# Performance work log

Hardware: AMD Instinct MI355X
Metric: run time of the kernel (lower is better)

The kernel has to match this reference:

```python
import jax, jax.numpy as jnp
import numpy as np
from jax.scipy.special import logsumexp

# K particles, J proposal candidates, N taxa, R merges done, T current subtrees,
# S sites, A alphabet, D embedding dim
K, J, N, R, T, S, A, D = 128, 4, 64, 32, 32, 256, 4, 64
PRIOR_BL = 0.1       # expected branch length under exponential prior
TEMPERATURE = 1.0


def _gather_nodes(arr, idx):
    # arr: (Z, t, ...); idx: (Z,) -> (Z, ...)  (per-row gather, gather_K)
    i = idx.reshape((-1,) + (1,) * (arr.ndim - 1))
    return jnp.take_along_axis(arr, i, axis=1)[:, 0]


def _replace_with_merged(arr, idx1, idx2, new_val):
    # remove nodes idx1, idx2 from each row (keeping order) and append merged node
    t = arr.shape[1]
    pos = jnp.arange(t)
    removed = (pos[None, :] == idx1[:, None]) | (pos[None, :] == idx2[:, None])
    order = jnp.argsort(removed.astype(jnp.int32), axis=1, stable=True)
    kept = order[:, : t - 2]
    ki = kept.reshape(kept.shape + (1,) * (arr.ndim - 2))
    kept_vals = jnp.take_along_axis(arr, ki, axis=1)
    return jnp.concatenate([kept_vals, new_val[:, None]], axis=1)


def _hash_tree(h1, h2):
    # order-invariant int32 hash combine (wraps on overflow, as intended)
    mn = jnp.minimum(h1, h2)
    mx = jnp.maximum(h1, h2)
    return (mn * 1000003 + mx) * 40503 + 2531011


def _q_matrix(emb_ZxD, W_q):
    # GTR-style rate matrix from merged-node embedding (site-independent decoder)
    logits = (emb_ZxD @ W_q).reshape(-1, A, A)
    off = jax.nn.softplus(logits) * (1.0 - jnp.eye(A, dtype=logits.dtype))
    return off - jnp.eye(A, dtype=logits.dtype) * off.sum(-1, keepdims=True)


def setup_inputs() -> dict:
    key = jax.random.key(0)
    ks = jax.random.split(key, 20)
    merge1_indexes_Kxr = jax.random.randint(ks[0], (K, R), 0, N).astype(jnp.int32)
    merge2_indexes_Kxr = jax.random.randint(ks[1], (K, R), 0, N).astype(jnp.int32)
    branch1_lengths_Kxr = jax.random.uniform(ks[2], (K, R)) * 0.2 + 1e-3
    branch2_lengths_Kxr = jax.random.uniform(ks[3], (K, R)) * 0.2 + 1e-3
    embeddings_KxrxD = jax.random.normal(ks[4], (K, R, D))
    # leaf counts per subtree, summing to N per particle
    lc_row = jnp.concatenate([jnp.full((T // 2,), 1, jnp.int32), jnp.full((T - T // 2,), 3, jnp.int32)])
    leaf_counts_Kxt = jnp.tile(lc_row[None], (K, 1))
    hashes_Kxt = jax.random.randint(ks[5], (K, T), 0, 2 ** 30).astype(jnp.int32)
    embeddings_KxtxD = jax.random.normal(ks[6], (K, T, D))
    log_felsensteins_KxtxSxA = -jax.random.uniform(ks[7], (K, T, S, A)) * 3.0
    log_pi_K = -jax.random.uniform(ks[8], (K,)) * 100.0
    indexes_K = jax.random.randint(ks[9], (K,), 0, K).astype(jnp.int32)
    # proposal outputs (stand-in for the learned proposal): idx1 != idx2
    idx1_KxJ = jax.random.randint(ks[10], (K, J), 0, T).astype(jnp.int32)
    off = jax.random.randint(ks[11], (K, J), 1, T).astype(jnp.int32)
    idx2_KxJ = (idx1_KxJ + off) % T
    branch1_KxJ = jax.random.uniform(ks[12], (K, J)) * 0.2 + 1e-3
    branch2_KxJ = jax.random.uniform(ks[13], (K, J)) * 0.2 + 1e-3
    embedding_KxJxD = jax.random.normal(ks[14], (K, J, D))
    log_v_plus_KxJ = jnp.full((K, J), np.log(T * (T - 1) / 2.0), jnp.float32)
    gumbel_KxJ = jax.random.gumbel(ks[15], (K, J))
    W_q = jax.random.normal(ks[16], (D, A * A)) * 0.05
    W_stat = jax.random.normal(ks[17], (D, A)) * 0.05
    vals = np.zeros(2 * N, dtype=np.float64)
    for i in range(2, 2 * N):
        vals[i] = vals[i - 2] + np.log(i)
    log_double_factorials_2N = jnp.asarray(vals, jnp.float32)
    return {
        'indexes_K': indexes_K,
        'merge1_indexes_Kxr': merge1_indexes_Kxr,
        'merge2_indexes_Kxr': merge2_indexes_Kxr,
        'branch1_lengths_Kxr': branch1_lengths_Kxr,
        'branch2_lengths_Kxr': branch2_lengths_Kxr,
        'embeddings_KxrxD': embeddings_KxrxD,
        'leaf_counts_Kxt': leaf_counts_Kxt,
        'hashes_Kxt': hashes_Kxt,
        'embeddings_KxtxD': embeddings_KxtxD,
        'log_felsensteins_KxtxSxA': log_felsensteins_KxtxSxA,
        'log_pi_K': log_pi_K,
        'idx1_KxJ': idx1_KxJ,
        'idx2_KxJ': idx2_KxJ,
        'branch1_KxJ': branch1_KxJ,
        'branch2_KxJ': branch2_KxJ,
        'embedding_KxJxD': embedding_KxJxD,
        'log_v_plus_KxJ': log_v_plus_KxJ,
        'gumbel_KxJ': gumbel_KxJ,
        'W_q': W_q,
        'W_stat': W_stat,
        'log_double_factorials_2N': log_double_factorials_2N,
    }


def reference(indexes_K, merge1_indexes_Kxr, merge2_indexes_Kxr,
              branch1_lengths_Kxr, branch2_lengths_Kxr, embeddings_KxrxD,
              leaf_counts_Kxt, hashes_Kxt, embeddings_KxtxD,
              log_felsensteins_KxtxSxA, log_pi_K,
              idx1_KxJ, idx2_KxJ, branch1_KxJ, branch2_KxJ,
              embedding_KxJxD, log_v_plus_KxJ, gumbel_KxJ,
              W_q, W_stat, log_double_factorials_2N):
    # ---- ancestor resampling gather (ms[...][indexes_K]) ----
    g = lambda a: a[indexes_K]
    merge1_Kxr = g(merge1_indexes_Kxr); merge2_Kxr = g(merge2_indexes_Kxr)
    b1_Kxr = g(branch1_lengths_Kxr); b2_Kxr = g(branch2_lengths_Kxr)
    emb_KxrxD = g(embeddings_KxrxD)
    lc_Kxt = g(leaf_counts_Kxt); h_Kxt = g(hashes_Kxt)
    emb_KxtxD = g(embeddings_KxtxD)
    lf_KxtxSxA = g(log_felsensteins_KxtxSxA)
    logpi_K = g(log_pi_K)
    # ---- flatten proposal to Z = K*J (hash_trick=False: Z = K*J, no dedup) ----
    Z = K * J
    rep = lambda a: jnp.repeat(a, J, axis=0)  # K_to_Z
    idx1_Z = idx1_KxJ.reshape(Z); idx2_Z = idx2_KxJ.reshape(Z)
    branch1_Z = branch1_KxJ.reshape(Z); branch2_Z = branch2_KxJ.reshape(Z)
    emb_ZxD = embedding_KxJxD.reshape(Z, D)
    log_v_plus_Z = log_v_plus_KxJ.reshape(Z)
    merge1_Z = rep(merge1_Kxr); merge2_Z = rep(merge2_Kxr)
    b1_Z = rep(b1_Kxr); b2_Z = rep(b2_Kxr)
    embr_Z = rep(emb_KxrxD)
    lc_Z = rep(lc_Kxt); h_Z = rep(h_Kxt)
    embt_Z = rep(emb_KxtxD)
    lf_Z = rep(lf_KxtxSxA)
    logpi_Z = rep(logpi_K)
    # ---- append candidate branches ----
    b1_all = jnp.concatenate([b1_Z, branch1_Z[:, None]], axis=1)  # Z x (R+1)
    b2_all = jnp.concatenate([b2_Z, branch2_Z[:, None]], axis=1)
    # ---- merge step ----
    new_lc = _gather_nodes(lc_Z, idx1_Z) + _gather_nodes(lc_Z, idx2_Z)
    new_h = _hash_tree(_gather_nodes(h_Z, idx1_Z), _gather_nodes(h_Z, idx2_Z))
    lc_new = _replace_with_merged(lc_Z, idx1_Z, idx2_Z, new_lc)      # Z x (T-1)
    h_new = _replace_with_merged(h_Z, idx1_Z, idx2_Z, new_h)
    embt_new = _replace_with_merged(embt_Z, idx1_Z, idx2_Z, emb_ZxD)
    # ---- Felsenstein pruning update ----
    Q = _q_matrix(emb_ZxD, W_q)                                      # Z x A x A
    expm = jax.scipy.linalg.expm
    P1 = jax.vmap(expm)(Q * branch1_Z[:, None, None])
    P2 = jax.vmap(expm)(Q * branch2_Z[:, None, None])
    logP1 = jnp.log(jnp.clip(P1, 1e-30))
    logP2 = jnp.log(jnp.clip(P2, 1e-30))
    lf1 = _gather_nodes(lf_Z, idx1_Z)  # Z x S x A
    lf2 = _gather_nodes(lf_Z, idx2_Z)
    new_lf = (logsumexp(logP1[:, None, :, :] + lf1[:, :, None, :], axis=-1)
              + logsumexp(logP2[:, None, :, :] + lf2[:, :, None, :], axis=-1))
    lf_new = _replace_with_merged(lf_Z, idx1_Z, idx2_Z, new_lf)      # Z x (T-1) x S x A
    # ---- stationary probs per node & log pi ----
    log_stat = jax.nn.log_softmax(embt_new @ W_stat, axis=-1)        # Z x (T-1) x A
    ll_nodes = logsumexp(lf_new + log_stat[:, :, None, :], axis=-1).sum(-1)  # Z x (T-1)
    log_lik_Z = ll_nodes.sum(-1)
    rate = 1.0 / PRIOR_BL
    log_branch_prior = ((jnp.log(rate) - rate * b1_all).sum(-1)
                        + (jnp.log(rate) - rate * b2_all).sum(-1))
    df_idx = jnp.clip(2 * lc_new - 3, 0, 2 * N - 1)
    log_topo = -log_double_factorials_2N[df_idx].sum(-1)
    log_pi_new_Z = log_lik_Z + log_branch_prior + log_topo
    log_v_minus_Z = jnp.log(jnp.sum(lc_new > 1, axis=-1).astype(jnp.float32))
    # ---- weights & sub-resampling ----
    log_w_Z = log_pi_new_Z - logpi_Z + log_v_minus_Z - log_v_plus_Z
    log_w_KxJ = log_w_Z.reshape(K, J)
    log_weight_K = logsumexp(log_w_KxJ, axis=1) - jnp.log(float(J))
    sub_idx_K = jnp.argmax(log_w_KxJ / TEMPERATURE + gumbel_KxJ, axis=1)  # Gumbel-max = Categorical sample
    sel = jnp.arange(K) * J + sub_idx_K
    gs = lambda a: a[sel]
    merge1_out = jnp.concatenate([gs(merge1_Z), gs(idx1_Z)[:, None]], axis=1)
    merge2_out = jnp.concatenate([gs(merge2_Z), gs(idx2_Z)[:, None]], axis=1)
    embr_out = jnp.concatenate([gs(embr_Z), gs(emb_ZxD)[:, None, :]], axis=1)
    return (merge1_out, merge2_out, gs(b1_all), gs(b2_all), embr_out,
            gs(lc_new), gs(h_new), gs(embt_new), gs(lf_new),
            gs(log_pi_new_Z), log_weight_K, gs(log_lik_Z))
```

## Files before the change

### kernel.cpp

```cpp
#include <hip/hip_runtime.h>
#include <math.h>

constexpr int K_ = 128, J_ = 4, R_ = 32, T_ = 32, S_ = 256, A_ = 4, D_ = 64;
constexpr int NDF_ = 128;
constexpr float RATE_ = 10.0f;

constexpr int OFF_M1   = 0;
constexpr int OFF_M2   = OFF_M1 + K_ * 33;
constexpr int OFF_B1   = OFF_M2 + K_ * 33;
constexpr int OFF_B2   = OFF_B1 + K_ * 33;
constexpr int OFF_EMBR = OFF_B2 + K_ * 33;
constexpr int OFF_LC   = OFF_EMBR + K_ * 33 * D_;
constexpr int OFF_H    = OFF_LC + K_ * 31;
constexpr int OFF_EMBT = OFF_H + K_ * 31;
constexpr int OFF_LF   = OFF_EMBT + K_ * 31 * D_;
constexpr int OFF_LPN  = OFF_LF + K_ * 31 * S_ * A_;
constexpr int OFF_LW   = OFF_LPN + K_;
constexpr int OFF_LL   = OFF_LW + K_;

__device__ inline float lse4f(float a, float b, float c, float d) {
    float m = fmaxf(fmaxf(a, b), fmaxf(c, d));
    return m + __logf(__expf(a - m) + __expf(b - m) + __expf(c - m) + __expf(d - m));
}

__global__ __launch_bounds__(256) void k_all(
    const int* __restrict__ indexes, const int* __restrict__ m1_Kr,
    const int* __restrict__ m2_Kr, const float* __restrict__ b1_Kr,
    const float* __restrict__ b2_Kr, const float* __restrict__ embr,
    const int* __restrict__ lc_Kt, const int* __restrict__ h_Kt,
    const float* __restrict__ embt, const float* __restrict__ lf,
    const float* __restrict__ logpi_K, const int* __restrict__ idx1_KJ,
    const int* __restrict__ idx2_KJ, const float* __restrict__ br1_KJ,
    const float* __restrict__ br2_KJ, const float* __restrict__ emb_KJD,
    const float* __restrict__ logvp_KJ, const float* __restrict__ gumbel_KJ,
    const float* __restrict__ Wq, const float* __restrict__ Wstat,
    const float* __restrict__ ldf, float* __restrict__ out) {
    int k = blockIdx.x;
    int tid = threadIdx.x;
    int w = tid >> 6, lane = tid & 63;
    int src = indexes[k];

    __shared__ float s_node_ll[T_];
    __shared__ float s_new_ll[J_];
    __shared__ float s_logP[J_][32];
    __shared__ int s_sub;

#pragma unroll
    for (int i = 0; i < 8; ++i) {
        int t = i * 4 + w;
        float e = embt[(src * T_ + t) * D_ + lane];
        const float4 w4 = *(const float4*)&Wstat[lane * 4];
        float g0 = e * w4.x, g1 = e * w4.y, g2 = e * w4.z, g3 = e * w4.w;
#pragma unroll
        for (int m = 32; m; m >>= 1) {
            g0 += __shfl_xor(g0, m, 64);
            g1 += __shfl_xor(g1, m, 64);
            g2 += __shfl_xor(g2, m, 64);
            g3 += __shfl_xor(g3, m, 64);
        }
        float lse = lse4f(g0, g1, g2, g3);
        float ls0 = g0 - lse, ls1 = g1 - lse, ls2 = g2 - lse, ls3 = g3 - lse;
        const float4* fr = (const float4*)&lf[(size_t)(src * T_ + t) * S_ * A_];
        double acc = 0.0;
#pragma unroll
        for (int s4 = 0; s4 < 4; ++s4) {
            float4 f = fr[s4 * 64 + lane];
            acc += (double)lse4f(f.x + ls0, f.y + ls1, f.z + ls2, f.w + ls3);
        }
#pragma unroll
        for (int m = 32; m; m >>= 1) acc += __shfl_xor(acc, m, 64);
        if (lane == 0) s_node_ll[t] = (float)acc;
    }

    {
        int z = k * J_ + w;
        int i1 = idx1_KJ[z], i2 = idx2_KJ[z];

        float emb_d = emb_KJD[z * D_ + lane];
        float lg[20];
        const float4* wqr = (const float4*)&Wq[lane * 16];
        float4 q0 = wqr[0], q1 = wqr[1], q2 = wqr[2], q3 = wqr[3];
        lg[0] = emb_d * q0.x;  lg[1] = emb_d * q0.y;  lg[2] = emb_d * q0.z;  lg[3] = emb_d * q0.w;
        lg[4] = emb_d * q1.x;  lg[5] = emb_d * q1.y;  lg[6] = emb_d * q1.z;  lg[7] = emb_d * q1.w;
        lg[8] = emb_d * q2.x;  lg[9] = emb_d * q2.y;  lg[10] = emb_d * q2.z; lg[11] = emb_d * q2.w;
        lg[12] = emb_d * q3.x; lg[13] = emb_d * q3.y; lg[14] = emb_d * q3.z; lg[15] = emb_d * q3.w;
        const float4 ws4 = *(const float4*)&Wstat[lane * 4];
        lg[16] = emb_d * ws4.x; lg[17] = emb_d * ws4.y; lg[18] = emb_d * ws4.z; lg[19] = emb_d * ws4.w;
#pragma unroll
        for (int m = 32; m; m >>= 1) {
#pragma unroll
            for (int p = 0; p < 20; ++p) lg[p] += __shfl_xor(lg[p], m, 64);
        }

        float lseS = lse4f(lg[16], lg[17], lg[18], lg[19]);
        float ls0 = lg[16] - lseS, ls1 = lg[17] - lseS, ls2 = lg[18] - lseS, ls3 = lg[19] - lseS;

        float lv[4] = {0.f, 0.f, 0.f, 0.f};
        if (lane < 8) {
            int h = lane >> 2, r = lane & 3, base = h * 4;
            float q[16];
#pragma unroll
            for (int i = 0; i < 4; ++i) {
                float rs = 0.f;
#pragma unroll
                for (int j = 0; j < 4; ++j) {
                    if (i != j) {
                        float x = lg[i * 4 + j];
                        float sp = (x > 15.f) ? x : log1pf(__expf(x));
                        q[i * 4 + j] = sp;
                        rs += sp;
                    }
                }
                q[i * 4 + i] = -rs;
            }
            float br = (h == 0) ? br1_KJ[z] : br2_KJ[z];
            float c = br * (1.f / 64.f);
#pragma unroll
            for (int e2 = 0; e2 < 16; ++e2) q[e2] *= c;
            float trow[4], arow[4];
#pragma unroll
            for (int j = 0; j < 4; ++j) { trow[j] = (j == r) ? 1.f : 0.f; arow[j] = trow[j]; }
            const float inv_n[11] = {0.f, 1.f, 0.5f, 1.f / 3.f, 0.25f, 0.2f,
                                     1.f / 6.f, 1.f / 7.f, 0.125f, 1.f / 9.f, 0.1f};
#pragma unroll
            for (int n = 1; n <= 10; ++n) {
                float nt[4];
#pragma unroll
                for (int j = 0; j < 4; ++j)
                    nt[j] = (trow[0] * q[0 * 4 + j] + trow[1] * q[1 * 4 + j] +
                             trow[2] * q[2 * 4 + j] + trow[3] * q[3 * 4 + j]) * inv_n[n];
#pragma unroll
                for (int j = 0; j < 4; ++j) { trow[j] = nt[j]; arow[j] += nt[j]; }
            }
#pragma unroll
            for (int sq = 0; sq < 6; ++sq) {
                float nrow[4];
#pragma unroll
                for (int j = 0; j < 4; ++j) {
                    float aj = arow[j];
                    nrow[j] = arow[0] * __shfl(aj, base + 0, 64)
                            + arow[1] * __shfl(aj, base + 1, 64)
                            + arow[2] * __shfl(aj, base + 2, 64)
                            + arow[3] * __shfl(aj, base + 3, 64);
                }
#pragma unroll
                for (int j = 0; j < 4; ++j) arow[j] = nrow[j];
            }
#pragma unroll
            for (int j = 0; j < 4; ++j) {
                lv[j] = __logf(fmaxf(arow[j], 1e-30f));
                s_logP[w][h * 16 + r * 4 + j] = lv[j];
            }
        }
        float p1[16], p2[16];
#pragma unroll
        for (int r = 0; r < 4; ++r) {
#pragma unroll
            for (int j = 0; j < 4; ++j) {
                p1[r * 4 + j] = __shfl(lv[j], r, 64);
                p2[r * 4 + j] = __shfl(lv[j], 4 + r, 64);
            }
        }
        const float4* f1p = (const float4*)&lf[(size_t)(src * T_ + i1) * S_ * A_];
        const float4* f2p = (const float4*)&lf[(size_t)(src * T_ + i2) * S_ * A_];
        double acc = 0.0;
#pragma unroll
        for (int s4 = 0; s4 < 4; ++s4) {
            float4 f = f1p[s4 * 64 + lane];
            float4 g = f2p[s4 * 64 + lane];
            float nlf[4];
#pragma unroll
            for (int a = 0; a < 4; ++a) {
                float t1 = lse4f(p1[a * 4 + 0] + f.x, p1[a * 4 + 1] + f.y,
                                 p1[a * 4 + 2] + f.z, p1[a * 4 + 3] + f.w);
                float t2 = lse4f(p2[a * 4 + 0] + g.x, p2[a * 4 + 1] + g.y,
                                 p2[a * 4 + 2] + g.z, p2[a * 4 + 3] + g.w);
                nlf[a] = t1 + t2;
            }
            acc += (double)lse4f(nlf[0] + ls0, nlf[1] + ls1, nlf[2] + ls2, nlf[3] + ls3);
        }
#pragma unroll
        for (int m = 32; m; m >>= 1) acc += __shfl_xor(acc, m, 64);
        if (lane == 0) s_new_ll[w] = (float)acc;
    }
    __syncthreads();

    if (w == 0) {
        double nll = 0.0, topo = 0.0, sb1 = 0.0, sb2 = 0.0;
        int cnt = 0;
        if (lane < T_) {
            nll = (double)s_node_ll[lane];
            int lc = lc_Kt[src * T_ + lane];
            int di = 2 * lc - 3; di = max(0, min(NDF_ - 1, di));
            topo = (double)ldf[di];
            cnt = (lc > 1) ? 1 : 0;
            sb1 = (double)b1_Kr[src * R_ + lane];
            sb2 = (double)b2_Kr[src * R_ + lane];
        }
        for (int o = 32; o > 0; o >>= 1) {
            nll += __shfl_down(nll, o, 64);
            topo += __shfl_down(topo, o, 64);
            sb1 += __shfl_down(sb1, o, 64);
            sb2 += __shfl_down(sb2, o, 64);
            cnt += __shfl_down(cnt, o, 64);
        }
        if (lane == 0) {
            double total_ll = nll, base_topo = -topo;
            const double lr = log(10.0);
            double lw[4], lpn[4], llik[4];
            for (int j = 0; j < J_; ++j) {
                int z = k * J_ + j;
                int i1 = idx1_KJ[z], i2 = idx2_KJ[z];
                int lc1 = lc_Kt[src * T_ + i1], lc2 = lc_Kt[src * T_ + i2];
                int nlc = lc1 + lc2;
                double loglik = total_ll - (double)s_node_ll[i1] - (double)s_node_ll[i2]
                              + (double)s_new_ll[j];
                double lbp = 66.0 * lr
                           - (double)RATE_ * (sb1 + (double)br1_KJ[z] + sb2 + (double)br2_KJ[z]);
                int d1 = max(0, min(NDF_ - 1, 2 * lc1 - 3));
                int d2 = max(0, min(NDF_ - 1, 2 * lc2 - 3));
                int dn = max(0, min(NDF_ - 1, 2 * nlc - 3));
                double lt = base_topo + (double)ldf[d1] + (double)ldf[d2] - (double)ldf[dn];
                int cntj = cnt - ((lc1 > 1) ? 1 : 0) - ((lc2 > 1) ? 1 : 0) + 1;
                double lvm = log((double)cntj);
                lpn[j] = loglik + lbp + lt;
                llik[j] = loglik;
                lw[j] = lpn[j] - (double)logpi_K[src] + lvm - (double)logvp_KJ[z];
            }
            double m = fmax(fmax(lw[0], lw[1]), fmax(lw[2], lw[3]));
            double ssum = exp(lw[0] - m) + exp(lw[1] - m) + exp(lw[2] - m) + exp(lw[3] - m);
            double logw = m + log(ssum) - log((double)J_);
            int best = 0;
            double bv = lw[0] + (double)gumbel_KJ[k * J_ + 0];
            for (int j = 1; j < J_; ++j) {
                double v = lw[j] + (double)gumbel_KJ[k * J_ + j];
                if (v > bv) { bv = v; best = j; }
            }
            out[OFF_LPN + k] = (float)lpn[best];
            out[OFF_LW + k] = (float)logw;
            out[OFF_LL + k] = (float)llik[best];
            s_sub = best;
        }
    }
    __syncthreads();

    int sub = s_sub;
    int zs = k * J_ + sub;
    int si1 = idx1_KJ[zs], si2 = idx2_KJ[zs];
    int mn = min(si1, si2), mx = max(si1, si2);

    {
        float P1[16], P2[16];
#pragma unroll
        for (int i = 0; i < 16; ++i) { P1[i] = s_logP[sub][i]; P2[i] = s_logP[sub][16 + i]; }
        const float4 f1 = *(const float4*)&lf[((size_t)(src * T_ + si1) * S_ + tid) * A_];
        const float4 f2 = *(const float4*)&lf[((size_t)(src * T_ + si2) * S_ + tid) * A_];
        float4 o4;
#pragma unroll
        for (int a = 0; a < 4; ++a) {
            float t1 = lse4f(P1[a * 4 + 0] + f1.x, P1[a * 4 + 1] + f1.y,
                             P1[a * 4 + 2] + f1.z, P1[a * 4 + 3] + f1.w);
            float t2 = lse4f(P2[a * 4 + 0] + f2.x, P2[a * 4 + 1] + f2.y,
                             P2[a * 4 + 2] + f2.z, P2[a * 4 + 3] + f2.w);
            ((float*)&o4)[a] = t1 + t2;
        }
        *(float4*)&out[OFF_LF + ((size_t)(k * 31 + 30) * S_ + tid) * A_] = o4;
    }
    for (int row = 0; row < 30; ++row) {
        int st = row;
        if (st >= mn) ++st;
        if (st >= mx) ++st;
        const float4 v = *(const float4*)&lf[((size_t)(src * T_ + st) * S_ + tid) * A_];
        *(float4*)&out[OFF_LF + ((size_t)(k * 31 + row) * S_ + tid) * A_] = v;
    }
    for (int i = tid; i < 33; i += 256) {
        float v1, v2, fb1, fb2;
        if (i < 32) {
            v1 = (float)m1_Kr[src * R_ + i];
            v2 = (float)m2_Kr[src * R_ + i];
            fb1 = b1_Kr[src * R_ + i];
            fb2 = b2_Kr[src * R_ + i];
        } else {
            v1 = (float)si1; v2 = (float)si2;
            fb1 = br1_KJ[zs]; fb2 = br2_KJ[zs];
        }
        out[OFF_M1 + k * 33 + i] = v1;
        out[OFF_M2 + k * 33 + i] = v2;
        out[OFF_B1 + k * 33 + i] = fb1;
        out[OFF_B2 + k * 33 + i] = fb2;
    }
    for (int i = tid; i < 33 * D_; i += 256) {
        int r = i >> 6, d = i & 63;
        float v = (r < 32) ? embr[(src * R_ + r) * D_ + d] : emb_KJD[zs * D_ + d];
        out[OFF_EMBR + k * 33 * D_ + i] = v;
    }
    for (int i = tid; i < 31; i += 256) {
        int lcv, hv;
        if (i < 30) {
            int st = i;
            if (st >= mn) ++st;
            if (st >= mx) ++st;
            lcv = lc_Kt[src * T_ + st];
            hv = h_Kt[src * T_ + st];
        } else {
            lcv = lc_Kt[src * T_ + si1] + lc_Kt[src * T_ + si2];
            int h1 = h_Kt[src * T_ + si1], h2 = h_Kt[src * T_ + si2];
            int hmn = min(h1, h2), hmx = max(h1, h2);
            unsigned int u = ((unsigned int)hmn * 1000003u + (unsigned int)hmx) * 40503u
                             + 2531011u;
            hv = (int)u;
        }
        out[OFF_LC + k * 31 + i] = (float)lcv;
        out[OFF_H + k * 31 + i] = (float)hv;
    }
    for (int i = tid; i < 31 * D_; i += 256) {
        int t = i >> 6, d = i & 63;
        float v;
        if (t < 30) {
            int st = t;
            if (st >= mn) ++st;
            if (st >= mx) ++st;
            v = embt[(src * T_ + st) * D_ + d];
        } else {
            v = emb_KJD[zs * D_ + d];
        }
        out[OFF_EMBT + k * 31 * D_ + i] = v;
    }
}

extern "C" void kernel_launch(void* const* d_in, const int* in_sizes, int n_in,
                              void* d_out, int out_size, void* d_ws, size_t ws_size,
                              hipStream_t stream) {
    const int* indexes   = (const int*)d_in[0];
    const int* m1_Kr     = (const int*)d_in[1];
    const int* m2_Kr     = (const int*)d_in[2];
    const float* b1_Kr   = (const float*)d_in[3];
    const float* b2_Kr   = (const float*)d_in[4];
    const float* embr    = (const float*)d_in[5];
    const int* lc_Kt     = (const int*)d_in[6];
    const int* h_Kt      = (const int*)d_in[7];
    const float* embt    = (const float*)d_in[8];
    const float* lf      = (const float*)d_in[9];
    const float* logpi_K = (const float*)d_in[10];
    const int* idx1_KJ   = (const int*)d_in[11];
    const int* idx2_KJ   = (const int*)d_in[12];
    const float* br1_KJ  = (const float*)d_in[13];
    const float* br2_KJ  = (const float*)d_in[14];
    const float* emb_KJD = (const float*)d_in[15];
    const float* logvp_KJ = (const float*)d_in[16];
    const float* gumbel_KJ = (const float*)d_in[17];
    const float* Wq      = (const float*)d_in[18];
    const float* Wstat   = (const float*)d_in[19];
    const float* ldf     = (const float*)d_in[20];
    float* out = (float*)d_out;

    k_all<<<K_, 256, 0, stream>>>(indexes, m1_Kr, m2_Kr, b1_Kr, b2_Kr, embr,
                                  lc_Kt, h_Kt, embt, lf, logpi_K, idx1_KJ, idx2_KJ,
                                  br1_KJ, br2_KJ, emb_KJD, logvp_KJ, gumbel_KJ,
                                  Wq, Wstat, ldf, out);
}
```

Baseline: 146.2 us.

## Split fused per-particle kernel into compute, finalize, and copy kernels with wider grids

Replaces the single 128-block kernel with three launches. A 9xK-block compute kernel spreads the node log-likelihoods and candidate evaluations across blocks and writes them to workspace. A small finalize kernel does the weight and Gumbel selection, and a 9xK-block copy kernel writes the gathered outputs with float4 accesses. The aim is to fill more compute units than the 128 blocks the old version used on a large GPU, at the cost of two extra launches and round trips through global workspace.

```diff
diff --git a/kernel.cpp b/kernel.cpp
--- a/kernel.cpp
+++ b/kernel.cpp
@@ -18,36 +18,30 @@
 constexpr int OFF_LW   = OFF_LPN + K_;
 constexpr int OFF_LL   = OFF_LW + K_;
 
+constexpr int WS_NODE  = 0;
+constexpr int WS_NEWLL = WS_NODE + K_ * T_;
+constexpr int WS_LOGP  = WS_NEWLL + K_ * J_;
+constexpr int WS_SUB   = WS_LOGP + K_ * J_ * 32;
+
 __device__ inline float lse4f(float a, float b, float c, float d) {
     float m = fmaxf(fmaxf(a, b), fmaxf(c, d));
     return m + __logf(__expf(a - m) + __expf(b - m) + __expf(c - m) + __expf(d - m));
 }
 
-__global__ __launch_bounds__(256) void k_all(
-    const int* __restrict__ indexes, const int* __restrict__ m1_Kr,
-    const int* __restrict__ m2_Kr, const float* __restrict__ b1_Kr,
-    const float* __restrict__ b2_Kr, const float* __restrict__ embr,
-    const int* __restrict__ lc_Kt, const int* __restrict__ h_Kt,
-    const float* __restrict__ embt, const float* __restrict__ lf,
-    const float* __restrict__ logpi_K, const int* __restrict__ idx1_KJ,
+__global__ __launch_bounds__(256) void k_compute(
+    const int* __restrict__ indexes, const float* __restrict__ embt,
+    const float* __restrict__ lf, const float* __restrict__ Wstat,
+    const float* __restrict__ Wq, const int* __restrict__ idx1_KJ,
     const int* __restrict__ idx2_KJ, const float* __restrict__ br1_KJ,
     const float* __restrict__ br2_KJ, const float* __restrict__ emb_KJD,
-    const float* __restrict__ logvp_KJ, const float* __restrict__ gumbel_KJ,
-    const float* __restrict__ Wq, const float* __restrict__ Wstat,
-    const float* __restrict__ ldf, float* __restrict__ out) {
-    int k = blockIdx.x;
-    int tid = threadIdx.x;
-    int w = tid >> 6, lane = tid & 63;
+    float* __restrict__ ws) {
+    int grp = blockIdx.x;
+    int k = blockIdx.y;
+    int tid = threadIdx.x, w = tid >> 6, lane = tid & 63;
     int src = indexes[k];
 
-    __shared__ float s_node_ll[T_];
-    __shared__ float s_new_ll[J_];
-    __shared__ float s_logP[J_][32];
-    __shared__ int s_sub;
-
-#pragma unroll
-    for (int i = 0; i < 8; ++i) {
-        int t = i * 4 + w;
+    if (grp < 8) {
+        int t = grp * 4 + w;
         float e = embt[(src * T_ + t) * D_ + lane];
         const float4 w4 = *(const float4*)&Wstat[lane * 4];
         float g0 = e * w4.x, g1 = e * w4.y, g2 = e * w4.z, g3 = e * w4.w;
@@ -69,10 +63,8 @@
         }
 #pragma unroll
         for (int m = 32; m; m >>= 1) acc += __shfl_xor(acc, m, 64);
-        if (lane == 0) s_node_ll[t] = (float)acc;
-    }
-
-    {
+        if (lane == 0) ws[WS_NODE + k * T_ + t] = (float)acc;
+    } else {
         int z = k * J_ + w;
         int i1 = idx1_KJ[z], i2 = idx2_KJ[z];
 
@@ -149,7 +141,7 @@
 #pragma unroll
             for (int j = 0; j < 4; ++j) {
                 lv[j] = __logf(fmaxf(arow[j], 1e-30f));
-                s_logP[w][h * 16 + r * 4 + j] = lv[j];
+                ws[WS_LOGP + z * 32 + h * 16 + r * 4 + j] = lv[j];
             }
         }
         float p1[16], p2[16];
@@ -167,113 +159,104 @@
 #pragma unroll
         for (int s4 = 0; s4 < 4; ++s4) {
             float4 f = f1p[s4 * 64 + lane];
-            float4 g = f2p[s4 * 64 + lane];
+            float4 f2v = f2p[s4 * 64 + lane];
             float nlf[4];
 #pragma unroll
             for (int a = 0; a < 4; ++a) {
                 float t1 = lse4f(p1[a * 4 + 0] + f.x, p1[a * 4 + 1] + f.y,
                                  p1[a * 4 + 2] + f.z, p1[a * 4 + 3] + f.w);
-                float t2 = lse4f(p2[a * 4 + 0] + g.x, p2[a * 4 + 1] + g.y,
-                                 p2[a * 4 + 2] + g.z, p2[a * 4 + 3] + g.w);
+                float t2 = lse4f(p2[a * 4 + 0] + f2v.x, p2[a * 4 + 1] + f2v.y,
+                                 p2[a * 4 + 2] + f2v.z, p2[a * 4 + 3] + f2v.w);
                 nlf[a] = t1 + t2;
             }
             acc += (double)lse4f(nlf[0] + ls0, nlf[1] + ls1, nlf[2] + ls2, nlf[3] + ls3);
         }
 #pragma unroll
         for (int m = 32; m; m >>= 1) acc += __shfl_xor(acc, m, 64);
-        if (lane == 0) s_new_ll[w] = (float)acc;
-    }
-    __syncthreads();
-
-    if (w == 0) {
-        double nll = 0.0, topo = 0.0, sb1 = 0.0, sb2 = 0.0;
-        int cnt = 0;
-        if (lane < T_) {
-            nll = (double)s_node_ll[lane];
-            int lc = lc_Kt[src * T_ + lane];
-            int di = 2 * lc - 3; di = max(0, min(NDF_ - 1, di));
-            topo = (double)ldf[di];
-            cnt = (lc > 1) ? 1 : 0;
-            sb1 = (double)b1_Kr[src * R_ + lane];
-            sb2 = (double)b2_Kr[src * R_ + lane];
-        }
-        for (int o = 32; o > 0; o >>= 1) {
-            nll += __shfl_down(nll, o, 64);
-            topo += __shfl_down(topo, o, 64);
-            sb1 += __shfl_down(sb1, o, 64);
-            sb2 += __shfl_down(sb2, o, 64);
-            cnt += __shfl_down(cnt, o, 64);
-        }
-        if (lane == 0) {
-            double total_ll = nll, base_topo = -topo;
-            const double lr = log(10.0);
-            double lw[4], lpn[4], llik[4];
-            for (int j = 0; j < J_; ++j) {
-                int z = k * J_ + j;
-                int i1 = idx1_KJ[z], i2 = idx2_KJ[z];
-                int lc1 = lc_Kt[src * T_ + i1], lc2 = lc_Kt[src * T_ + i2];
-                int nlc = lc1 + lc2;
-                double loglik = total_ll - (double)s_node_ll[i1] - (double)s_node_ll[i2]
-                              + (double)s_new_ll[j];
-                double lbp = 66.0 * lr
-                           - (double)RATE_ * (sb1 + (double)br1_KJ[z] + sb2 + (double)br2_KJ[z]);
-                int d1 = max(0, min(NDF_ - 1, 2 * lc1 - 3));
-                int d2 = max(0, min(NDF_ - 1, 2 * lc2 - 3));
-                int dn = max(0, min(NDF_ - 1, 2 * nlc - 3));
-                double lt = base_topo + (double)ldf[d1] + (double)ldf[d2] - (double)ldf[dn];
-                int cntj = cnt - ((lc1 > 1) ? 1 : 0) - ((lc2 > 1) ? 1 : 0) + 1;
-                double lvm = log((double)cntj);
-                lpn[j] = loglik + lbp + lt;
-                llik[j] = loglik;
-                lw[j] = lpn[j] - (double)logpi_K[src] + lvm - (double)logvp_KJ[z];
-            }
-            double m = fmax(fmax(lw[0], lw[1]), fmax(lw[2], lw[3]));
-            double ssum = exp(lw[0] - m) + exp(lw[1] - m) + exp(lw[2] - m) + exp(lw[3] - m);
-            double logw = m + log(ssum) - log((double)J_);
-            int best = 0;
-            double bv = lw[0] + (double)gumbel_KJ[k * J_ + 0];
-            for (int j = 1; j < J_; ++j) {
-                double v = lw[j] + (double)gumbel_KJ[k * J_ + j];
-                if (v > bv) { bv = v; best = j; }
-            }
-            out[OFF_LPN + k] = (float)lpn[best];
-            out[OFF_LW + k] = (float)logw;
-            out[OFF_LL + k] = (float)llik[best];
-            s_sub = best;
-        }
-    }
-    __syncthreads();
-
-    int sub = s_sub;
-    int zs = k * J_ + sub;
+        if (lane == 0) ws[WS_NEWLL + z] = (float)acc;
+    }
+}
+
+__global__ __launch_bounds__(64) void k_finalize(
+    const int* __restrict__ indexes, const int* __restrict__ m1_Kr,
+    const int* __restrict__ m2_Kr, const float* __restrict__ b1_Kr,
+    const float* __restrict__ b2_Kr, const int* __restrict__ lc_Kt,
+    const int* __restrict__ h_Kt, const float* __restrict__ logpi_K,
+    const int* __restrict__ idx1_KJ, const int* __restrict__ idx2_KJ,
+    const float* __restrict__ br1_KJ, const float* __restrict__ br2_KJ,
+    const float* __restrict__ logvp_KJ, const float* __restrict__ gumbel_KJ,
+    const float* __restrict__ ldf, float* __restrict__ ws, float* __restrict__ out) {
+    int k = blockIdx.x;
+    int lane = threadIdx.x;
+    int src = indexes[k];
+
+    double nll = 0.0, topo = 0.0, sb1 = 0.0, sb2 = 0.0;
+    int cnt = 0;
+    if (lane < T_) {
+        nll = (double)ws[WS_NODE + k * T_ + lane];
+        int lc = lc_Kt[src * T_ + lane];
+        int di = 2 * lc - 3; di = max(0, min(NDF_ - 1, di));
+        topo = (double)ldf[di];
+        cnt = (lc > 1) ? 1 : 0;
+        sb1 = (double)b1_Kr[src * R_ + lane];
+        sb2 = (double)b2_Kr[src * R_ + lane];
+    }
+    for (int o = 32; o > 0; o >>= 1) {
+        nll += __shfl_down(nll, o, 64);
+        topo += __shfl_down(topo, o, 64);
+        sb1 += __shfl_down(sb1, o, 64);
+        sb2 += __shfl_down(sb2, o, 64);
+        cnt += __shfl_down(cnt, o, 64);
+    }
+    nll = __shfl(nll, 0, 64); topo = __shfl(topo, 0, 64);
+    sb1 = __shfl(sb1, 0, 64); sb2 = __shfl(sb2, 0, 64);
+    cnt = __shfl(cnt, 0, 64);
+    double total_ll = nll, base_topo = -topo;
+    const double lr = log(10.0);
+
+    double lwj = 0.0, lpnj = 0.0, llikj = 0.0;
+    if (lane < J_) {
+        int j = lane, z = k * J_ + j;
+        int i1 = idx1_KJ[z], i2 = idx2_KJ[z];
+        int lc1 = lc_Kt[src * T_ + i1], lc2 = lc_Kt[src * T_ + i2];
+        int nlc = lc1 + lc2;
+        double loglik = total_ll - (double)ws[WS_NODE + k * T_ + i1]
+                      - (double)ws[WS_NODE + k * T_ + i2] + (double)ws[WS_NEWLL + z];
+        double lbp = 66.0 * lr
+                   - (double)RATE_ * (sb1 + (double)br1_KJ[z] + sb2 + (double)br2_KJ[z]);
+        int d1 = max(0, min(NDF_ - 1, 2 * lc1 - 3));
+        int d2 = max(0, min(NDF_ - 1, 2 * lc2 - 3));
+        int dn = max(0, min(NDF_ - 1, 2 * nlc - 3));
+        double lt = base_topo + (double)ldf[d1] + (double)ldf[d2] - (double)ldf[dn];
+        int cntj = cnt - ((lc1 > 1) ? 1 : 0) - ((lc2 > 1) ? 1 : 0) + 1;
+        double lvm = log((double)cntj);
+        lpnj = loglik + lbp + lt;
+        llikj = loglik;
+        lwj = lpnj - (double)logpi_K[src] + lvm - (double)logvp_KJ[z];
+    }
+    double lw0 = __shfl(lwj, 0, 64), lw1 = __shfl(lwj, 1, 64);
+    double lw2 = __shfl(lwj, 2, 64), lw3 = __shfl(lwj, 3, 64);
+    double m = fmax(fmax(lw0, lw1), fmax(lw2, lw3));
+    double ssum = exp(lw0 - m) + exp(lw1 - m) + exp(lw2 - m) + exp(lw3 - m);
+    double logw = m + log(ssum) - log((double)J_);
+    int best = 0;
+    double bv = lw0 + (double)gumbel_KJ[k * J_ + 0];
+    { double v = lw1 + (double)gumbel_KJ[k * J_ + 1]; if (v > bv) { bv = v; best = 1; } }
+    { double v = lw2 + (double)gumbel_KJ[k * J_ + 2]; if (v > bv) { bv = v; best = 2; } }
+    { double v = lw3 + (double)gumbel_KJ[k * J_ + 3]; if (v > bv) { bv = v; best = 3; } }
+    double lpn_b = __shfl(lpnj, best, 64);
+    double llik_b = __shfl(llikj, best, 64);
+    if (lane == 0) {
+        out[OFF_LPN + k] = (float)lpn_b;
+        out[OFF_LW + k] = (float)logw;
+        out[OFF_LL + k] = (float)llik_b;
+        ((int*)(ws + WS_SUB))[k] = best;
+    }
+
+    int zs = k * J_ + best;
     int si1 = idx1_KJ[zs], si2 = idx2_KJ[zs];
     int mn = min(si1, si2), mx = max(si1, si2);
-
-    {
-        float P1[16], P2[16];
-#pragma unroll
-        for (int i = 0; i < 16; ++i) { P1[i] = s_logP[sub][i]; P2[i] = s_logP[sub][16 + i]; }
-        const float4 f1 = *(const float4*)&lf[((size_t)(src * T_ + si1) * S_ + tid) * A_];
-        const float4 f2 = *(const float4*)&lf[((size_t)(src * T_ + si2) * S_ + tid) * A_];
-        float4 o4;
-#pragma unroll
-        for (int a = 0; a < 4; ++a) {
-            float t1 = lse4f(P1[a * 4 + 0] + f1.x, P1[a * 4 + 1] + f1.y,
-                             P1[a * 4 + 2] + f1.z, P1[a * 4 + 3] + f1.w);
-            float t2 = lse4f(P2[a * 4 + 0] + f2.x, P2[a * 4 + 1] + f2.y,
-                             P2[a * 4 + 2] + f2.z, P2[a * 4 + 3] + f2.w);
-            ((float*)&o4)[a] = t1 + t2;
-        }
-        *(float4*)&out[OFF_LF + ((size_t)(k * 31 + 30) * S_ + tid) * A_] = o4;
-    }
-    for (int row = 0; row < 30; ++row) {
-        int st = row;
-        if (st >= mn) ++st;
-        if (st >= mx) ++st;
-        const float4 v = *(const float4*)&lf[((size_t)(src * T_ + st) * S_ + tid) * A_];
-        *(float4*)&out[OFF_LF + ((size_t)(k * 31 + row) * S_ + tid) * A_] = v;
-    }
-    for (int i = tid; i < 33; i += 256) {
+    for (int i = lane; i < 33; i += 64) {
         float v1, v2, fb1, fb2;
         if (i < 32) {
             v1 = (float)m1_Kr[src * R_ + i];
@@ -289,12 +272,7 @@
         out[OFF_B1 + k * 33 + i] = fb1;
         out[OFF_B2 + k * 33 + i] = fb2;
     }
-    for (int i = tid; i < 33 * D_; i += 256) {
-        int r = i >> 6, d = i & 63;
-        float v = (r < 32) ? embr[(src * R_ + r) * D_ + d] : emb_KJD[zs * D_ + d];
-        out[OFF_EMBR + k * 33 * D_ + i] = v;
-    }
-    for (int i = tid; i < 31; i += 256) {
+    for (int i = lane; i < 31; i += 64) {
         int lcv, hv;
         if (i < 30) {
             int st = i;
@@ -313,18 +291,77 @@
         out[OFF_LC + k * 31 + i] = (float)lcv;
         out[OFF_H + k * 31 + i] = (float)hv;
     }
-    for (int i = tid; i < 31 * D_; i += 256) {
-        int t = i >> 6, d = i & 63;
-        float v;
-        if (t < 30) {
-            int st = t;
-            if (st >= mn) ++st;
-            if (st >= mx) ++st;
-            v = embt[(src * T_ + st) * D_ + d];
-        } else {
-            v = emb_KJD[zs * D_ + d];
-        }
-        out[OFF_EMBT + k * 31 * D_ + i] = v;
+}
+
+__global__ __launch_bounds__(256) void k_copy(
+    const int* __restrict__ indexes, const int* __restrict__ idx1_KJ,
+    const int* __restrict__ idx2_KJ, const float* __restrict__ embr,
+    const float* __restrict__ embt, const float* __restrict__ lf,
+    const float* __restrict__ emb_KJD, const float* __restrict__ ws,
+    float* __restrict__ out) {
+    int grp = blockIdx.x;
+    int k = blockIdx.y;
+    int tid = threadIdx.x;
+    int src = indexes[k];
+    int sub = ((const int*)(ws + WS_SUB))[k];
+    int zs = k * J_ + sub;
+    int si1 = idx1_KJ[zs], si2 = idx2_KJ[zs];
+    int mn = min(si1, si2), mx = max(si1, si2);
+
+    if (grp < 8) {
+        __shared__ float sP[32];
+        if (grp == 7) {
+            if (tid < 32) sP[tid] = ws[WS_LOGP + zs * 32 + tid];
+            __syncthreads();
+        }
+#pragma unroll
+        for (int rr = 0; rr < 4; ++rr) {
+            int row = grp * 4 + rr;
+            if (row >= 31) break;
+            if (row < 30) {
+                int st = row;
+                if (st >= mn) ++st;
+                if (st >= mx) ++st;
+                const float4 v = *(const float4*)&lf[((size_t)(src * T_ + st) * S_ + tid) * A_];
+                *(float4*)&out[OFF_LF + ((size_t)(k * 31 + row) * S_ + tid) * A_] = v;
+            } else {
+                float P1[16], P2[16];
+#pragma unroll
+                for (int i = 0; i < 16; ++i) { P1[i] = sP[i]; P2[i] = sP[16 + i]; }
+                const float4 f1 = *(const float4*)&lf[((size_t)(src * T_ + si1) * S_ + tid) * A_];
+                const float4 f2 = *(const float4*)&lf[((size_t)(src * T_ + si2) * S_ + tid) * A_];
+                float4 o4;
+#pragma unroll
+                for (int a = 0; a < 4; ++a) {
+                    float t1 = lse4f(P1[a * 4 + 0] + f1.x, P1[a * 4 + 1] + f1.y,
+                                     P1[a * 4 + 2] + f1.z, P1[a * 4 + 3] + f1.w);
+                    float t2 = lse4f(P2[a * 4 + 0] + f2.x, P2[a * 4 + 1] + f2.y,
+                                     P2[a * 4 + 2] + f2.z, P2[a * 4 + 3] + f2.w);
+                    ((float*)&o4)[a] = t1 + t2;
+                }
+                *(float4*)&out[OFF_LF + ((size_t)(k * 31 + 30) * S_ + tid) * A_] = o4;
+            }
+        }
+    } else {
+        for (int i = tid; i < 33 * 16; i += 256) {
+            int r = i >> 4, c = i & 15;
+            float4 v = (r < 32) ? *(const float4*)&embr[(src * R_ + r) * D_ + c * 4]
+                                : *(const float4*)&emb_KJD[zs * D_ + c * 4];
+            *(float4*)&out[OFF_EMBR + k * 33 * D_ + i * 4] = v;
+        }
+        for (int i = tid; i < 31 * 16; i += 256) {
+            int t = i >> 4, c = i & 15;
+            float4 v;
+            if (t < 30) {
+                int st = t;
+                if (st >= mn) ++st;
+                if (st >= mx) ++st;
+                v = *(const float4*)&embt[(src * T_ + st) * D_ + c * 4];
+            } else {
+                v = *(const float4*)&emb_KJD[zs * D_ + c * 4];
+            }
+            *(float4*)&out[OFF_EMBT + k * 31 * D_ + i * 4] = v;
+        }
     }
 }
 
@@ -353,9 +390,15 @@
     const float* Wstat   = (const float*)d_in[19];
     const float* ldf     = (const float*)d_in[20];
     float* out = (float*)d_out;
-
-    k_all<<<K_, 256, 0, stream>>>(indexes, m1_Kr, m2_Kr, b1_Kr, b2_Kr, embr,
-                                  lc_Kt, h_Kt, embt, lf, logpi_K, idx1_KJ, idx2_KJ,
-                                  br1_KJ, br2_KJ, emb_KJD, logvp_KJ, gumbel_KJ,
-                                  Wq, Wstat, ldf, out);
+    float* ws = (float*)d_ws;
+
+    k_compute<<<dim3(9, K_), 256, 0, stream>>>(indexes, embt, lf, Wstat, Wq,
+                                               idx1_KJ, idx2_KJ, br1_KJ, br2_KJ,
+                                               emb_KJD, ws);
+    k_finalize<<<K_, 64, 0, stream>>>(indexes, m1_Kr, m2_Kr, b1_Kr, b2_Kr,
+                                      lc_Kt, h_Kt, logpi_K, idx1_KJ, idx2_KJ,
+                                      br1_KJ, br2_KJ, logvp_KJ, gumbel_KJ,
+                                      ldf, ws, out);
+    k_copy<<<dim3(9, K_), 256, 0, stream>>>(indexes, idx1_KJ, idx2_KJ, embr,
+                                            embt, lf, emb_KJD, ws, out);
 }
```

Result: faster. 132.8 us (-9.2%).

## Split bulk partial-likelihood row copy into a separate wide-grid kernel

Applied to the files above, without the earlier changes.

The 30-row copy of kept partial likelihoods per particle moves out of the single 128-block kernel into a second kernel with a grid of 8x128 blocks, each copying up to four rows. The chosen sub-index is passed from the first kernel through workspace memory. The aim is to spread the bandwidth-bound copy across more blocks than the 128 particles, at the cost of an extra launch and a serial dependency between the two kernels.

```diff
diff --git a/kernel.cpp b/kernel.cpp
--- a/kernel.cpp
+++ b/kernel.cpp
@@ -18,12 +18,13 @@
 constexpr int OFF_LW   = OFF_LPN + K_;
 constexpr int OFF_LL   = OFF_LW + K_;
 
+
 __device__ inline float lse4f(float a, float b, float c, float d) {
     float m = fmaxf(fmaxf(a, b), fmaxf(c, d));
     return m + __logf(__expf(a - m) + __expf(b - m) + __expf(c - m) + __expf(d - m));
 }
 
-__global__ __launch_bounds__(256) void k_all(
+__global__ __launch_bounds__(256) void k_main(
     const int* __restrict__ indexes, const int* __restrict__ m1_Kr,
     const int* __restrict__ m2_Kr, const float* __restrict__ b1_Kr,
     const float* __restrict__ b2_Kr, const float* __restrict__ embr,
@@ -34,7 +35,8 @@
     const float* __restrict__ br2_KJ, const float* __restrict__ emb_KJD,
     const float* __restrict__ logvp_KJ, const float* __restrict__ gumbel_KJ,
     const float* __restrict__ Wq, const float* __restrict__ Wstat,
-    const float* __restrict__ ldf, float* __restrict__ out) {
+    const float* __restrict__ ldf, int* __restrict__ ws_sub,
+    float* __restrict__ out) {
     int k = blockIdx.x;
     int tid = threadIdx.x;
     int w = tid >> 6, lane = tid & 63;
@@ -240,6 +242,7 @@
             out[OFF_LW + k] = (float)logw;
             out[OFF_LL + k] = (float)llik[best];
             s_sub = best;
+            ws_sub[k] = best;
         }
     }
     __syncthreads();
@@ -265,13 +268,6 @@
             ((float*)&o4)[a] = t1 + t2;
         }
         *(float4*)&out[OFF_LF + ((size_t)(k * 31 + 30) * S_ + tid) * A_] = o4;
-    }
-    for (int row = 0; row < 30; ++row) {
-        int st = row;
-        if (st >= mn) ++st;
-        if (st >= mx) ++st;
-        const float4 v = *(const float4*)&lf[((size_t)(src * T_ + st) * S_ + tid) * A_];
-        *(float4*)&out[OFF_LF + ((size_t)(k * 31 + row) * S_ + tid) * A_] = v;
     }
     for (int i = tid; i < 33; i += 256) {
         float v1, v2, fb1, fb2;
@@ -325,6 +321,31 @@
             v = emb_KJD[zs * D_ + d];
         }
         out[OFF_EMBT + k * 31 * D_ + i] = v;
+    }
+}
+
+__global__ __launch_bounds__(256) void k_copy(
+    const int* __restrict__ indexes, const int* __restrict__ idx1_KJ,
+    const int* __restrict__ idx2_KJ, const float* __restrict__ lf,
+    const int* __restrict__ ws_sub, float* __restrict__ out) {
+    int grp = blockIdx.x;
+    int k = blockIdx.y;
+    int tid = threadIdx.x;
+    int src = indexes[k];
+    int sub = ws_sub[k];
+    int zs = k * J_ + sub;
+    int si1 = idx1_KJ[zs], si2 = idx2_KJ[zs];
+    int mn = min(si1, si2), mx = max(si1, si2);
+
+#pragma unroll
+    for (int rr = 0; rr < 4; ++rr) {
+        int row = grp * 4 + rr;
+        if (row >= 30) break;
+        int st = row;
+        if (st >= mn) ++st;
+        if (st >= mx) ++st;
+        const float4 v = *(const float4*)&lf[((size_t)(src * T_ + st) * S_ + tid) * A_];
+        *(float4*)&out[OFF_LF + ((size_t)(k * 31 + row) * S_ + tid) * A_] = v;
     }
 }
 
@@ -353,9 +374,12 @@
     const float* Wstat   = (const float*)d_in[19];
     const float* ldf     = (const float*)d_in[20];
     float* out = (float*)d_out;
-
-    k_all<<<K_, 256, 0, stream>>>(indexes, m1_Kr, m2_Kr, b1_Kr, b2_Kr, embr,
-                                  lc_Kt, h_Kt, embt, lf, logpi_K, idx1_KJ, idx2_KJ,
-                                  br1_KJ, br2_KJ, emb_KJD, logvp_KJ, gumbel_KJ,
-                                  Wq, Wstat, ldf, out);
+    int* ws_sub = (int*)d_ws;
+
+    k_main<<<K_, 256, 0, stream>>>(indexes, m1_Kr, m2_Kr, b1_Kr, b2_Kr, embr,
+                                   lc_Kt, h_Kt, embt, lf, logpi_K, idx1_KJ,
+                                   idx2_KJ, br1_KJ, br2_KJ, emb_KJD, logvp_KJ,
+                                   gumbel_KJ, Wq, Wstat, ldf, ws_sub, out);
+    k_copy<<<dim3(8, K_), 256, 0, stream>>>(indexes, idx1_KJ, idx2_KJ, lf,
+                                            ws_sub, out);
 }
```

Result: no change. 145.3 us (-0.7%).
